# Performance work log

Hardware: AMD Instinct MI355X
Metric: run time of the kernel (lower is better)

## Reference

```python
import jax, jax.numpy as jnp
import numpy as np

N = 100000
E = 1600000
D = 128  # in_dim == out_dim


def setup_inputs() -> dict:
    key = jax.random.key(0)
    k1, k2, k3, k4, k5 = jax.random.split(key, 5)
    x = jax.random.normal(k1, (N, D), dtype=jnp.float32)
    edge_index = jax.random.randint(k2, (2, E), 0, N, dtype=jnp.int64)
    edge_attr = jax.random.normal(k3, (E, 8), dtype=jnp.float32)
    # nn.Linear(in_dim, out_dim) params: W [out, in], b [out]
    bound = 1.0 / np.sqrt(D)
    W = jax.random.uniform(k4, (D, D), minval=-bound, maxval=bound, dtype=jnp.float32)
    b = jax.random.uniform(k5, (D,), minval=-bound, maxval=bound, dtype=jnp.float32)
    return {"x": x, "edge_index": edge_index, "edge_attr": edge_attr, "W": W, "b": b}


def reference(x, edge_index, edge_attr, W, b):
    row, col = edge_index[0], edge_index[1]
    # gather neighbor features then scatter-add into destination rows
    agg = jax.ops.segment_sum(x[col], row, num_segments=x.shape[0])  # [N, D]
    h = (x + agg) @ W.T + b  # linear
    return jax.nn.silu(h)
```

## Files before the change

kernel.cpp:

```cpp
#include <hip/hip_runtime.h>
#include <math.h>

#define NN 100000
#define NE 1600000
#define DD 128
#define CAP 64

typedef short bf16x8 __attribute__((ext_vector_type(8)));
typedef float f32x4  __attribute__((ext_vector_type(4)));
typedef int   i32x2  __attribute__((ext_vector_type(2)));

__device__ inline float bf2f(unsigned short u) {
    unsigned int v = ((unsigned int)u) << 16;
    return __uint_as_float(v);
}
__device__ inline unsigned short f2bf(float f) {
    unsigned int u = __float_as_uint(f);
    unsigned int r = (u + 0x7FFFu + ((u >> 16) & 1u)) >> 16;
    return (unsigned short)r;
}

__global__ void f2bf_kernel(const float* __restrict__ src,
                            unsigned short* __restrict__ dst, int n4) {
    int i = blockIdx.x * blockDim.x + threadIdx.x;
    if (i >= n4) return;
    float4 v = ((const float4*)src)[i];
    ushort4 o;
    o.x = f2bf(v.x); o.y = f2bf(v.y); o.z = f2bf(v.z); o.w = f2bf(v.w);
    ((ushort4*)dst)[i] = o;
}

__global__ void zero_cnt_kernel(int* cnt) {
    int i = blockIdx.x * blockDim.x + threadIdx.x;
    if (i < NN) cnt[i] = 0;
}

#define FILL_CHUNK 6250
__global__ __launch_bounds__(256)
void fill_kernel(const int* __restrict__ eidx,
                 int* __restrict__ cnt,
                 int* __restrict__ slot) {
    const int bucket = blockIdx.x & 7;
    const int chunk  = blockIdx.x >> 3;
    const int lo     = bucket * 12500;
    const int base   = chunk * FILL_CHUNK;

    const i32x2* r2 = (const i32x2*)(eidx + base);
    for (int i = threadIdx.x; i < FILL_CHUNK / 2; i += 256) {
        const i32x2 rr = __builtin_nontemporal_load(&r2[i]);
        const int e0 = base + 2 * i;
        if ((unsigned)(rr.x - lo) < 12500u) {
            const int c = __builtin_nontemporal_load(&eidx[NE + e0]);
            const int pos = atomicAdd(&cnt[rr.x], 1);
            if (pos < CAP) slot[(rr.x << 6) + pos] = c;
        }
        if ((unsigned)(rr.y - lo) < 12500u) {
            const int c = __builtin_nontemporal_load(&eidx[NE + e0 + 1]);
            const int pos = atomicAdd(&cnt[rr.y], 1);
            if (pos < CAP) slot[(rr.y << 6) + pos] = c;
        }
    }
}

__global__ __launch_bounds__(256)
void gather_kernel(const unsigned short* __restrict__ x16,
                   const int* __restrict__ cnt,
                   const int* __restrict__ slot,
                   unsigned short* __restrict__ V16) {
    const int lane = threadIdx.x & 15;
    const int node = (int)((blockIdx.x * 256u + threadIdx.x) >> 4);
    if (node >= NN) return;
    const bf16x8* xv = (const bf16x8*)x16;

    bf16x8 s = xv[(size_t)node * 16 + lane];
    float a[8];
    #pragma unroll
    for (int k = 0; k < 8; ++k) a[k] = bf2f((unsigned short)s[k]);

    int deg = cnt[node];
    if (deg > CAP) deg = CAP;
    const int base = node << 6;

    for (int d = 0; d < deg; d += 8) {
        const int4 c0 = *(const int4*)&slot[base + d];
        const int4 c1 = *(const int4*)&slot[base + d + 4];
        int idx[8] = {c0.x, c0.y, c0.z, c0.w, c1.x, c1.y, c1.z, c1.w};
        float w[8];
        #pragma unroll
        for (int j = 0; j < 8; ++j) {
            const bool live = (d + j) < deg;
            w[j] = live ? 1.f : 0.f;
            if (!live) idx[j] = node;
        }
        bf16x8 t[8];
        #pragma unroll
        for (int j = 0; j < 8; ++j) t[j] = xv[(size_t)idx[j] * 16 + lane];
        #pragma unroll
        for (int j = 0; j < 8; ++j) {
            #pragma unroll
            for (int k = 0; k < 8; ++k)
                a[k] = fmaf(w[j], bf2f((unsigned short)t[j][k]), a[k]);
        }
    }

    bf16x8 o;
    #pragma unroll
    for (int k = 0; k < 8; ++k) o[k] = (short)f2bf(a[k]);
    ((bf16x8*)V16)[(size_t)node * 16 + lane] = o;
}

__global__ __launch_bounds__(256)
void gemm_mfma_kernel(const unsigned short* __restrict__ V16,
                      const unsigned short* __restrict__ W16,
                      const float* __restrict__ bias,
                      float* __restrict__ out) {
    const int wave = threadIdx.x >> 6;
    const int lane = threadIdx.x & 63;
    const int strip = blockIdx.x * 4 + wave;
    if (strip >= NN / 16) return;
    const int m0 = strip << 4;
    const int r = lane & 15;
    const int q = lane >> 4;

    const bf16x8* Arow = (const bf16x8*)(V16 + (size_t)(m0 + r) * 128);
    bf16x8 a[4];
    #pragma unroll
    for (int kk = 0; kk < 4; ++kk) a[kk] = Arow[kk * 4 + q];

    f32x4 acc[8];
    #pragma unroll
    for (int n = 0; n < 8; ++n) acc[n] = (f32x4){0.f, 0.f, 0.f, 0.f};

    #pragma unroll
    for (int kk = 0; kk < 4; ++kk) {
        #pragma unroll
        for (int n = 0; n < 8; ++n) {
            const bf16x8 b =
                ((const bf16x8*)(W16 + (size_t)(n * 16 + r) * 128))[kk * 4 + q];
            acc[n] = __builtin_amdgcn_mfma_f32_16x16x32_bf16(a[kk], b, acc[n], 0, 0, 0);
        }
    }

    #pragma unroll
    for (int n = 0; n < 8; ++n) {
        const int col = n * 16 + r;
        const float bv = bias[col];
        #pragma unroll
        for (int i = 0; i < 4; ++i) {
            const int row = m0 + q * 4 + i;
            float h = acc[n][i] + bv;
            h = h / (1.f + __expf(-h));
            out[(size_t)row * 128 + col] = h;
        }
    }
}

extern "C" void kernel_launch(void* const* d_in, const int* in_sizes, int n_in,
                              void* d_out, int out_size, void* d_ws, size_t ws_size,
                              hipStream_t stream) {
    const float* x    = (const float*)d_in[0];
    const int*   eidx = (const int*)d_in[1];
    const float* W    = (const float*)d_in[3];
    const float* b    = (const float*)d_in[4];
    float* out = (float*)d_out;

    char* ws = (char*)d_ws;
    int*            cnt  = (int*)(ws);
    int*            slot = (int*)(ws + (512u << 10));
    unsigned short* x16  = (unsigned short*)(ws + (26u << 20));
    unsigned short* V16  = (unsigned short*)(ws + (51u << 20));
    unsigned short* W16  = (unsigned short*)(ws + (76u << 20));

    zero_cnt_kernel<<<(NN + 255) / 256, 256, 0, stream>>>(cnt);
    fill_kernel<<<8 * 256, 256, 0, stream>>>(eidx, cnt, slot);
    f2bf_kernel<<<(NN * DD / 4 + 255) / 256, 256, 0, stream>>>(x, x16, NN * DD / 4);
    f2bf_kernel<<<(DD * DD / 4 + 255) / 256, 256, 0, stream>>>(W, W16, DD * DD / 4);
    gather_kernel<<<(NN * 16 + 255) / 256, 256, 0, stream>>>(x16, cnt, slot, V16);
    gemm_mfma_kernel<<<(NN / 16 + 3) / 4, 256, 0, stream>>>(V16, W16, b, out);
}
```

Baseline: 317.7 us.

## Partition edges into per-chunk bucket queues before scattering into adjacency slots

The old fill kernel made each of 8 bucket blocks re-read the whole row chunk and filter it. The new code adds a partition pass that reads every edge once. It bins each (col,row) pair into shared-counter queues per chunk and bucket, stored in workspace that aliases the V16 buffer. A scatter kernel then replays each queue, doing the per-node atomics and slot writes. This removes the 8x redundant index reads but adds an extra write and read of packed 64-bit pairs, an extra launch, and a fixed QCAP that can drop edges if a bucket overflows.

```diff
diff --git a/kernel.cpp b/kernel.cpp
--- a/kernel.cpp
+++ b/kernel.cpp
@@ -6,9 +6,12 @@
 #define DD 128
 #define CAP 64
 
+#define NB    512
+#define CHUNK 3125
+#define QCAP  768
+
 typedef short bf16x8 __attribute__((ext_vector_type(8)));
 typedef float f32x4  __attribute__((ext_vector_type(4)));
-typedef int   i32x2  __attribute__((ext_vector_type(2)));
 
 __device__ inline float bf2f(unsigned short u) {
     unsigned int v = ((unsigned int)u) << 16;
@@ -35,30 +38,46 @@
     if (i < NN) cnt[i] = 0;
 }
 
-#define FILL_CHUNK 6250
-__global__ __launch_bounds__(256)
-void fill_kernel(const int* __restrict__ eidx,
-                 int* __restrict__ cnt,
-                 int* __restrict__ slot) {
+__global__ __launch_bounds__(256)
+void partition_kernel(const int* __restrict__ eidx,
+                      unsigned long long* __restrict__ q,
+                      int* __restrict__ qn) {
+    __shared__ int qc[8];
+    if (threadIdx.x < 8) qc[threadIdx.x] = 0;
+    __syncthreads();
+    const int base = blockIdx.x * CHUNK;
+    for (int i = threadIdx.x; i < CHUNK; i += 256) {
+        const int e = base + i;
+        const int r = __builtin_nontemporal_load(&eidx[e]);
+        const int c = __builtin_nontemporal_load(&eidx[NE + e]);
+        const int b = r / 12500;
+        const int pos = atomicAdd(&qc[b], 1);
+        if (pos < QCAP)
+            q[((size_t)blockIdx.x * 8 + b) * QCAP + pos] =
+                ((unsigned long long)(unsigned)c << 32) | (unsigned)r;
+    }
+    __syncthreads();
+    if (threadIdx.x < 8) {
+        int v = qc[threadIdx.x]; if (v > QCAP) v = QCAP;
+        qn[blockIdx.x * 8 + threadIdx.x] = v;
+    }
+}
+
+__global__ __launch_bounds__(256)
+void scatter_kernel(const unsigned long long* __restrict__ q,
+                    const int* __restrict__ qn,
+                    int* __restrict__ cnt,
+                    int* __restrict__ slot) {
     const int bucket = blockIdx.x & 7;
     const int chunk  = blockIdx.x >> 3;
-    const int lo     = bucket * 12500;
-    const int base   = chunk * FILL_CHUNK;
-
-    const i32x2* r2 = (const i32x2*)(eidx + base);
-    for (int i = threadIdx.x; i < FILL_CHUNK / 2; i += 256) {
-        const i32x2 rr = __builtin_nontemporal_load(&r2[i]);
-        const int e0 = base + 2 * i;
-        if ((unsigned)(rr.x - lo) < 12500u) {
-            const int c = __builtin_nontemporal_load(&eidx[NE + e0]);
-            const int pos = atomicAdd(&cnt[rr.x], 1);
-            if (pos < CAP) slot[(rr.x << 6) + pos] = c;
-        }
-        if ((unsigned)(rr.y - lo) < 12500u) {
-            const int c = __builtin_nontemporal_load(&eidx[NE + e0 + 1]);
-            const int pos = atomicAdd(&cnt[rr.y], 1);
-            if (pos < CAP) slot[(rr.y << 6) + pos] = c;
-        }
+    const int n = qn[chunk * 8 + bucket];
+    const unsigned long long* qq = q + ((size_t)chunk * 8 + bucket) * QCAP;
+    for (int i = threadIdx.x; i < n; i += 256) {
+        const unsigned long long p = qq[i];
+        const int r = (int)(p & 0xffffffffu);
+        const int c = (int)(p >> 32);
+        const int pos = atomicAdd(&cnt[r], 1);
+        if (pos < CAP) slot[(r << 6) + pos] = c;
     }
 }
 
@@ -166,13 +185,16 @@
 
     char* ws = (char*)d_ws;
     int*            cnt  = (int*)(ws);
+    int*            qn   = (int*)(ws + (448u << 10));
     int*            slot = (int*)(ws + (512u << 10));
     unsigned short* x16  = (unsigned short*)(ws + (26u << 20));
     unsigned short* V16  = (unsigned short*)(ws + (51u << 20));
     unsigned short* W16  = (unsigned short*)(ws + (76u << 20));
+    unsigned long long* q = (unsigned long long*)(ws + (51u << 20));
 
     zero_cnt_kernel<<<(NN + 255) / 256, 256, 0, stream>>>(cnt);
-    fill_kernel<<<8 * 256, 256, 0, stream>>>(eidx, cnt, slot);
+    partition_kernel<<<NB, 256, 0, stream>>>(eidx, q, qn);
+    scatter_kernel<<<8 * NB, 256, 0, stream>>>(q, qn, cnt, slot);
     f2bf_kernel<<<(NN * DD / 4 + 255) / 256, 256, 0, stream>>>(x, x16, NN * DD / 4);
     f2bf_kernel<<<(DD * DD / 4 + 255) / 256, 256, 0, stream>>>(W, W16, DD * DD / 4);
     gather_kernel<<<(NN * 16 + 255) / 256, 256, 0, stream>>>(x16, cnt, slot, V16);
```

Result: slower. 329.4 us (+3.7%).
